# Performance work log

Measured on AMD Instinct MI355X. Metric: run time of the kernel, lower is better.

Reference implementation:

```python
import jax, jax.numpy as jnp
import numpy as np

N_TASK, N_RET, N_DRAM, N_LINK = 50000, 20000, 5000, 100000
E_RET, E_DRAM, E_LINK = 1_000_000, 250_000, 2_000_000
H = 64


def setup_inputs() -> dict:
    key = jax.random.key(0)
    k = jax.random.split(key, 17)
    s = 1.0 / np.sqrt(3 * H)
    return {
        "feat_ret":  jax.random.normal(k[0], (E_RET, 1), jnp.float32),
        "feat_dram": jax.random.normal(k[1], (E_DRAM, 1), jnp.float32),
        "feat_link": jax.random.normal(k[2], (E_LINK, 1), jnp.float32),
        "W_ret":  jax.random.normal(k[3], (H, 1), jnp.float32),
        "b_ret":  jax.random.normal(k[4], (H,), jnp.float32) * 0.1,
        "W_dram": jax.random.normal(k[5], (H, 1), jnp.float32),
        "b_dram": jax.random.normal(k[6], (H,), jnp.float32) * 0.1,
        "W_link": jax.random.normal(k[7], (H, 1), jnp.float32),
        "b_link": jax.random.normal(k[8], (H,), jnp.float32) * 0.1,
        "W_task": jax.random.normal(k[9], (H, 3 * H), jnp.float32) * s,
        "b_task": jax.random.normal(k[10], (H,), jnp.float32) * 0.1,
        "task_ret":  jax.random.randint(k[11], (E_RET,), 0, N_TASK),
        "mod_ret":   jax.random.randint(k[12], (E_RET,), 0, N_RET),
        "task_dram": jax.random.randint(k[13], (E_DRAM,), 0, N_TASK),
        "mod_dram":  jax.random.randint(k[14], (E_DRAM,), 0, N_DRAM),
        "task_link": jax.random.randint(k[15], (E_LINK,), 0, N_TASK),
        "mod_link":  jax.random.randint(k[16], (E_LINK,), 0, N_LINK),
    }


def _gather_inp(feat, mod_idx, n_mod, W, b):
    # use_X: copy_e('feat') + sum per module node, then Linear(1,H) + tanh (activate_inp)
    inp = jax.ops.segment_sum(feat, mod_idx, num_segments=n_mod)  # [n_mod, 1]
    return jnp.tanh(inp @ W.T + b)                                # [n_mod, H]


def _max_to_task(inp_mod, mod_idx, task_idx, n_task):
    # X_used_by: copy_u('inp') + max per task node; zero-in-degree tasks -> 0 (DGL convention)
    m = jax.ops.segment_max(inp_mod[mod_idx], task_idx, num_segments=n_task)
    deg = jax.ops.segment_sum(jnp.ones_like(task_idx), task_idx, num_segments=n_task)
    return jnp.where((deg > 0)[:, None], m, 0.0)


def reference(feat_ret, feat_dram, feat_link, W_ret, b_ret, W_dram, b_dram,
              W_link, b_link, W_task, b_task,
              task_ret, mod_ret, task_dram, mod_dram, task_link, mod_link):
    # _module_update_inp
    inp_ret  = _gather_inp(feat_ret,  mod_ret,  N_RET,  W_ret,  b_ret)
    inp_dram = _gather_inp(feat_dram, mod_dram, N_DRAM, W_dram, b_dram)
    inp_link = _gather_inp(feat_link, mod_link, N_LINK, W_link, b_link)

    # _task_update_h: per-etype max reduce, cross-etype concat, Linear(3H,H) + tanh
    h_cat = jnp.concatenate([
        _max_to_task(inp_ret,  mod_ret,  task_ret,  N_TASK),
        _max_to_task(inp_dram, mod_dram, task_dram, N_TASK),
        _max_to_task(inp_link, mod_link, task_link, N_TASK),
    ], axis=-1)                                                   # [N_TASK, 3H]
    h_task = jnp.tanh(h_cat @ W_task.T + b_task)                  # [N_TASK, H]

    # _module_update_h: use_link copy_u('h') + mean per link node
    s = jax.ops.segment_sum(h_task[task_link], mod_link, num_segments=N_LINK)
    deg = jax.ops.segment_sum(jnp.ones((E_LINK,), jnp.float32), mod_link, num_segments=N_LINK)
    h_link = jnp.where((deg > 0)[:, None], s / jnp.maximum(deg, 1.0)[:, None], 0.0)
    return h_link
```

## Files before the change

kernel.cpp:

```cpp
#include <hip/hip_runtime.h>
#include <stdint.h>

#define N_TASK 50000
#define N_RET 20000
#define N_DRAM 5000
#define N_LINK 100000
#define E_RET 1000000
#define E_DRAM 250000
#define E_LINK 2000000

#define SBE 4096
#define NS_RET 245
#define NS_DRAM 62
#define NS_LINK 489
#define NS_TOT (NS_RET + NS_DRAM + NS_LINK)
#define MR_RET 64
#define RSZ_RET 313
#define MR_DRAM 16
#define RSZ_DRAM 313
#define MR_LINK 256
#define RSZ_LINK 391
#define RECIP313 107203u
#define RECIP391 85817u
#define CAPM_RET 16250
#define CAPM_DRAM 16250
#define CAPM_LINK 8255
#define BM4_RET 0
#define BM4_DRAM (MR_RET * NS_RET)
#define BM4_LINK (BM4_DRAM + MR_DRAM * NS_DRAM)
#define BM4_TOT (BM4_LINK + MR_LINK * NS_LINK)
#define BT_RET 0
#define BT_DRAM (16 * NS_RET)
#define BT_LINK (BT_DRAM + 16 * NS_DRAM)
#define BT_TOT (BT_LINK + 16 * NS_LINK)

#define R_PART 3125
#define CAP_RET 63800
#define CAP_DRAM 16300
#define CAP_LINK 126800
#define SUB_RET 4
#define SUB_DRAM 1
#define SUB_LINK 8
#define PB_RET 0
#define PB_DRAM (16 * SUB_RET * R_PART)
#define PB_LINK (PB_DRAM + 16 * SUB_DRAM * R_PART)
#define PB_TOT (PB_LINK + 16 * SUB_LINK * R_PART)

#define WS_SRET 0
#define WS_SDRAM 80000
#define WS_SLINK 100000
#define WS_CNT 500000
#define WS_OFFS 900000
#define WS_TMAX 1300000
#define WS_TMIN 1900000
#define WS_BCNT 2500000
#define WS_RCNT 2500192
#define WS_CSR 2501536
#define WS_BLKM 10501536
#define WS_BLKB 11068960
#define WS_MREC_RET 15701536
#define WS_MREC_DRAM 24021536
#define WS_MREC_LINK 26101536
#define WS_PART1 15701536
#define WS_HPL0_1 20901536
#define WS_HPL1_1 24101536
#define WS_TREC32_RET 43007776
#define WS_TREC32_DRAM 47090976
#define WS_TREC32_LINK 48134176
#define WS_WTB_1 56249376
#define WS_NEED1 56273952
#define WS_PART2 10501536
#define WS_TREC_RET 15701536
#define WS_TREC_DRAM 23867936
#define WS_TREC_LINK 25954336
#define WS_HPL0_2 15701536
#define WS_HPL1_2 18901536
#define WS_WTB_2 43007776
#define WS_NEED2 43032352

#define MS_STAGE 16512

typedef __attribute__((ext_vector_type(8))) short bf16x8;
typedef __attribute__((ext_vector_type(4))) float f32x4;
typedef unsigned long long u64;

__device__ __forceinline__ unsigned ford(float f) {
  unsigned u = __float_as_uint(f);
  return (u & 0x80000000u) ? ~u : (u | 0x80000000u);
}
__device__ __forceinline__ float funord(unsigned t) {
  unsigned u = (t & 0x80000000u) ? (t & 0x7fffffffu) : ~t;
  return __uint_as_float(u);
}
__device__ __forceinline__ unsigned short bf16rne(float f) {
  unsigned u = __float_as_uint(f);
  return (unsigned short)((u + 0x7fffu + ((u >> 16) & 1u)) >> 16);
}

__device__ __forceinline__ int wscan64(int v, int lane) {
#pragma unroll
  for (int d = 1; d < 64; d <<= 1) {
    int x = __shfl_up(v, d, 64);
    if (lane >= d) v += x;
  }
  return v;
}

__device__ __forceinline__ void decode_sblk(int bx, int& e, int& blk, int& E0, int& NB,
                                            int& NR, unsigned& RECIP, int& RSZ, int& base) {
  if (bx < NS_RET) {
    e = 0; blk = bx; E0 = E_RET; NB = NS_RET; NR = MR_RET; RECIP = RECIP313; RSZ = RSZ_RET; base = BM4_RET;
  } else if (bx < NS_RET + NS_DRAM) {
    e = 1; blk = bx - NS_RET; E0 = E_DRAM; NB = NS_DRAM; NR = MR_DRAM; RECIP = RECIP313; RSZ = RSZ_DRAM; base = BM4_DRAM;
  } else {
    e = 2; blk = bx - NS_RET - NS_DRAM; E0 = E_LINK; NB = NS_LINK; NR = MR_LINK; RECIP = RECIP391; RSZ = RSZ_LINK; base = BM4_LINK;
  }
}
__device__ __forceinline__ void decode_stblk(int bx, int& e, int& blk, int& E0, int& NB,
                                             int& baset) {
  if (bx < NS_RET) { e = 0; blk = bx; E0 = E_RET; NB = NS_RET; baset = BT_RET; }
  else if (bx < NS_RET + NS_DRAM) { e = 1; blk = bx - NS_RET; E0 = E_DRAM; NB = NS_DRAM; baset = BT_DRAM; }
  else { e = 2; blk = bx - NS_RET - NS_DRAM; E0 = E_LINK; NB = NS_LINK; baset = BT_LINK; }
}


__global__ __launch_bounds__(256) void k_count3(
    const int* __restrict__ mr, const int* __restrict__ md, const int* __restrict__ ml,
    const float* __restrict__ W_task, unsigned short* __restrict__ wtb,
    int* __restrict__ blkcnt_m, int* __restrict__ tcur) {
  int bx = blockIdx.x, tid = threadIdx.x;
  if (bx == NS_TOT + 48) {
    if (tid < 48) tcur[tid] = 0;
    return;
  }
  if (bx >= NS_TOT) {
    int i = (bx - NS_TOT) * 256 + tid;
    if (i < 64 * 192) wtb[i] = bf16rne(W_task[i]);
    return;
  }
  __shared__ int c[256];
  int e, blk, E0, NB, NR, RSZ, base; unsigned RECIP;
  decode_sblk(bx, e, blk, E0, NB, NR, RECIP, RSZ, base);
  const int* mod = (e == 0) ? mr : (e == 1) ? md : ml;
  c[tid] = 0;
  __syncthreads();
  int i0 = blk * SBE;
#pragma unroll
  for (int q = 0; q < 16; q++) {
    int i = i0 + q * 256 + tid;
    if (i < E0) {
      int m = mod[i];
      int r = (int)(((u64)(unsigned)m * RECIP) >> 25);
      atomicAdd(&c[r], 1);
    }
  }
  __syncthreads();
  for (int r = tid; r < NR; r += 256)
    blkcnt_m[base + r * NB + blk] = c[r];
}

__global__ __launch_bounds__(512) void k_scan3(const int* __restrict__ blkcnt_m,
                                               int* __restrict__ blkbase_m,
                                               int* __restrict__ rcnt) {
  __shared__ int wred[8];
  int gb = blockIdx.x, tid = threadIdx.x;
  int lane = tid & 63, w = tid >> 6;
  int NB, off;
  if (gb < 64) { NB = NS_RET; off = BM4_RET + gb * NS_RET; }
  else if (gb < 80) { NB = NS_DRAM; off = BM4_DRAM + (gb - 64) * NS_DRAM; }
  else { NB = NS_LINK; off = BM4_LINK + (gb - 80) * NS_LINK; }
  int v = (tid < NB) ? blkcnt_m[off + tid] : 0;
  int incl = wscan64(v, lane);
  if (lane == 63) wred[w] = incl;
  __syncthreads();
  if (tid < 8) {
    int x = wred[tid];
#pragma unroll
    for (int d = 1; d < 8; d <<= 1) {
      int t = __shfl_up(x, d, 8);
      if ((tid & 7) >= d) x += t;
    }
    wred[tid] = x;
  }
  __syncthreads();
  int base = (w > 0) ? wred[w - 1] : 0;
  incl += base;
  if (tid < NB) blkbase_m[off + tid] = incl - v;
  if (tid == 511) rcnt[gb] = incl;
}

__global__ __launch_bounds__(512) void k_mscatter3(
    const int* __restrict__ mr, const int* __restrict__ md, const int* __restrict__ ml,
    const int* __restrict__ tr, const int* __restrict__ td, const int* __restrict__ tl,
    const float* __restrict__ fr, const float* __restrict__ fd, const float* __restrict__ fl,
    const int* __restrict__ blkcnt_m, const int* __restrict__ blkbase_m,
    u64* __restrict__ mrec_ret, u64* __restrict__ mrec_dram, u64* __restrict__ mrec_link) {
  __shared__ int lcur[256];
  __shared__ int pdelta[256];
  __shared__ int wred[4];
  __shared__ u64 srec[SBE];
  __shared__ int sdelta[SBE];
  int tid = threadIdx.x;
  int lane = tid & 63, w = tid >> 6;
  int e, blk, E0, NB, NR, RSZ, base; unsigned RECIP;
  decode_sblk(blockIdx.x, e, blk, E0, NB, NR, RECIP, RSZ, base);
  const int* mod = (e == 0) ? mr : (e == 1) ? md : ml;
  const int* task = (e == 0) ? tr : (e == 1) ? td : tl;
  const float* feat = (e == 0) ? fr : (e == 1) ? fd : fl;
  u64* out = (e == 0) ? mrec_ret : (e == 1) ? mrec_dram : mrec_link;
  int CAP = (e == 0) ? CAPM_RET : (e == 1) ? CAPM_DRAM : CAPM_LINK;
  int cnt_r = 0, base_r = 0;
  if (tid < NR) {
    cnt_r = blkcnt_m[base + tid * NB + blk];
    base_r = blkbase_m[base + tid * NB + blk];
  }
  int incl = 0;
  if (tid < 256) incl = wscan64(cnt_r, lane);
  if (tid < 256 && lane == 63) wred[w] = incl;
  __syncthreads();
  if (tid < 4) {
    int x = wred[tid];
#pragma unroll
    for (int d = 1; d < 4; d <<= 1) {
      int t = __shfl_up(x, d, 4);
      if ((tid & 3) >= d) x += t;
    }
    wred[tid] = x;
  }
  __syncthreads();
  if (tid < 256) {
    int wb = (w > 0) ? wred[w - 1] : 0;
    int excl = incl + wb - cnt_r;
    lcur[tid] = excl;
    pdelta[tid] = tid * CAP + base_r - excl;
  }
  __syncthreads();
  int i0 = blk * SBE;
#pragma unroll
  for (int q = 0; q < 8; q++) {
    int i = i0 + q * 512 + tid;
    if (i < E0) {
      int m = mod[i];
      int r = (int)(((u64)(unsigned)m * RECIP) >> 25);
      unsigned mloc = (unsigned)(m - r * RSZ);
      unsigned tk = (unsigned)task[i];
      unsigned fu = __float_as_uint(feat[i]);
      int slot = atomicAdd(&lcur[r], 1);
      srec[slot] = ((u64)fu << 32) | (tk << 16) | mloc;
      int gpos = pdelta[r] + slot - r * CAP;
      sdelta[slot] = (gpos < CAP) ? pdelta[r] : (int)0x80000000;
    }
  }
  __syncthreads();
  int total = E0 - i0; if (total > SBE) total = SBE;
  for (int s = tid; s < total; s += 512) {
    int d = sdelta[s];
    if (d != (int)0x80000000) out[d + s] = srec[s];
  }
}

#define P1BODY(rec, moff) { \
  int mloc_ = (int)((rec) & 0xFFFFull) + (moff); \
  int task_ = (int)(((rec) >> 16) & 0xFFFFull); \
  atomicAdd(&ssum[mloc_], __uint_as_float((unsigned)((rec) >> 32))); \
  if (e == 2) atomicAdd(&scnt[mloc_], 1); \
  atomicAdd(&tcnt4[w][task_ / R_PART][s4], 1); }

#define P3BODY(rec, moff) { \
  int mloc_ = (int)((rec) & 0xFFFFull) + (moff); \
  int task_ = (int)(((rec) >> 16) & 0xFFFFull); \
  if (e == 2) { int lp_ = atomicAdd(&soff[mloc_], 1); scsr2[lp_] = (unsigned short)task_; } \
  int b_ = task_ / R_PART; \
  unsigned tl12_ = (unsigned)(task_ - b_ * R_PART); \
  unsigned u_ = (ford(ssum[mloc_]) & 0xFFFFF000u) | tl12_; \
  int local_ = atomicAdd(&tcnt4[w][b_][s4], 1); \
  strec[lbase[b_] + tbase4[w][b_][s4] + local_] = u_; }

__global__ __launch_bounds__(1024) void k_msum3(
    const u64* __restrict__ mrec_ret, const u64* __restrict__ mrec_dram,
    const u64* __restrict__ mrec_link, const int* __restrict__ rcnt,
    int* __restrict__ cnt, int* __restrict__ offs, unsigned short* __restrict__ csr,
    int* __restrict__ tcur,
    unsigned* __restrict__ trec_ret, unsigned* __restrict__ trec_dram,
    unsigned* __restrict__ trec_link) {
  __shared__ float ssum[2 * RSZ_LINK];
  __shared__ int scnt[2 * RSZ_LINK];
  __shared__ int soff[2 * RSZ_LINK + 1];
  __shared__ int tcnt4[16][16][4];
  __shared__ int tbase4[16][16][4];
  __shared__ int g0s[16], tot16[16], lbase[16];
  __shared__ int wred[17];
  __shared__ unsigned strec[MS_STAGE];
  __shared__ unsigned short scsr2[MS_STAGE];
  int gb = blockIdx.x, tid = threadIdx.x;
  int w = tid >> 6, lane = tid & 63, s4 = tid & 3;
  int e, m0, nmod, RSZtot, CAPT, rl0 = 0;
  int cnt0, cnt1 = 0;
  const u64 *p0, *p1 = nullptr;
  unsigned* trec;
  if (gb < MR_RET) {
    e = 0; p0 = mrec_ret + (long)gb * CAPM_RET;
    cnt0 = rcnt[gb]; if (cnt0 > CAPM_RET) cnt0 = CAPM_RET;
    RSZtot = RSZ_RET; m0 = gb * RSZ_RET; nmod = N_RET - m0;
    CAPT = CAP_RET; trec = trec_ret;
  } else if (gb < MR_RET + MR_DRAM) {
    e = 1; int rl = gb - MR_RET; p0 = mrec_dram + (long)rl * CAPM_DRAM;
    cnt0 = rcnt[gb]; if (cnt0 > CAPM_DRAM) cnt0 = CAPM_DRAM;
    RSZtot = RSZ_DRAM; m0 = rl * RSZ_DRAM; nmod = N_DRAM - m0;
    CAPT = CAP_DRAM; trec = trec_dram;
  } else {
    e = 2; rl0 = 2 * (gb - (MR_RET + MR_DRAM));
    p0 = mrec_link + (long)rl0 * CAPM_LINK; p1 = p0 + CAPM_LINK;
    cnt0 = rcnt[80 + rl0]; if (cnt0 > CAPM_LINK) cnt0 = CAPM_LINK;
    cnt1 = rcnt[80 + rl0 + 1]; if (cnt1 > CAPM_LINK) cnt1 = CAPM_LINK;
    RSZtot = 2 * RSZ_LINK; m0 = rl0 * RSZ_LINK; nmod = N_LINK - m0;
    CAPT = CAP_LINK; trec = trec_link;
  }
  if (nmod > RSZtot) nmod = RSZtot;
  for (int j = tid; j < RSZtot; j += 1024) { ssum[j] = 0.f; scnt[j] = 0; }
  ((int*)tcnt4)[tid] = 0;
  __syncthreads();
  {
    int i = tid;
    for (; i + 3072 < cnt0; i += 4096) {
      u64 a = p0[i], b = p0[i + 1024], c = p0[i + 2048], d = p0[i + 3072];
      P1BODY(a, 0) P1BODY(b, 0) P1BODY(c, 0) P1BODY(d, 0)
    }
    for (; i < cnt0; i += 1024) { u64 a = p0[i]; P1BODY(a, 0) }
    if (e == 2) {
      i = tid;
      for (; i + 3072 < cnt1; i += 4096) {
        u64 a = p1[i], b = p1[i + 1024], c = p1[i + 2048], d = p1[i + 3072];
        P1BODY(a, RSZ_LINK) P1BODY(b, RSZ_LINK) P1BODY(c, RSZ_LINK) P1BODY(d, RSZ_LINK)
      }
      for (; i < cnt1; i += 1024) { u64 a = p1[i]; P1BODY(a, RSZ_LINK) }
    }
  }
  __syncthreads();
  if (tid < 16) {
    int b2 = tid, run = 0;
    for (int w2 = 0; w2 < 16; w2++) {
#pragma unroll
      for (int s = 0; s < 4; s++) { tbase4[w2][b2][s] = run; run += tcnt4[w2][b2][s]; }
    }
    tot16[b2] = run;
    g0s[b2] = atomicAdd(&tcur[e * 16 + b2], run);
  }
  __syncthreads();
  ((int*)tcnt4)[tid] = 0;
  if (tid == 0) {
    int run = 0;
    for (int b2 = 0; b2 < 16; b2++) { lbase[b2] = run; run += tot16[b2]; }
  }
  int rb = 0;
  if (e == 2) {
    int part = (tid < 256 && tid < rl0) ? rcnt[80 + tid] : 0;
#pragma unroll
    for (int d = 1; d < 64; d <<= 1) part += __shfl_xor(part, d, 64);
    if (tid < 256 && lane == 0) wred[w] = part;
    __syncthreads();
    if (tid == 0) wred[16] = wred[0] + wred[1] + wred[2] + wred[3];
    __syncthreads();
    rb = wred[16];
    int vv = (tid < nmod) ? scnt[tid] : 0;
    int incl = wscan64(vv, lane);
    if (lane == 63) wred[w] = incl;
    __syncthreads();
    if (tid < 16) {
      int x = wred[tid];
#pragma unroll
      for (int d = 1; d < 16; d <<= 1) {
        int t = __shfl_up(x, d, 16);
        if ((tid & 15) >= d) x += t;
      }
      wred[tid] = x;
    }
    __syncthreads();
    int wb = (w > 0) ? wred[w - 1] : 0;
    incl += wb;
    if (tid < nmod) soff[tid] = incl - vv;
    __syncthreads();
    for (int j = tid; j < nmod; j += 1024) {
      cnt[m0 + j] = scnt[j];
      offs[m0 + j] = rb + soff[j];
    }
  }
  __syncthreads();
  {
    int i = tid;
    for (; i + 3072 < cnt0; i += 4096) {
      u64 a = p0[i], b = p0[i + 1024], c = p0[i + 2048], d = p0[i + 3072];
      P3BODY(a, 0) P3BODY(b, 0) P3BODY(c, 0) P3BODY(d, 0)
    }
    for (; i < cnt0; i += 1024) { u64 a = p0[i]; P3BODY(a, 0) }
    if (e == 2) {
      i = tid;
      for (; i + 3072 < cnt1; i += 4096) {
        u64 a = p1[i], b = p1[i + 1024], c = p1[i + 2048], d = p1[i + 3072];
        P3BODY(a, RSZ_LINK) P3BODY(b, RSZ_LINK) P3BODY(c, RSZ_LINK) P3BODY(d, RSZ_LINK)
      }
      for (; i < cnt1; i += 1024) { u64 a = p1[i]; P3BODY(a, RSZ_LINK) }
    }
  }
  __syncthreads();
  for (int b = 0; b < 16; b++) {
    int g0b = g0s[b];
    int kmax = tot16[b];
    int rem = CAPT - g0b; if (rem < 0) rem = 0;
    if (kmax > rem) kmax = rem;
    unsigned* dst = trec + (long)b * CAPT + g0b;
    const unsigned* src = strec + lbase[b];
    for (int k = tid; k < kmax; k += 1024) dst[k] = src[k];
  }
  if (e == 2) {
    int ctot = cnt0 + cnt1;
    for (int k = tid; k < ctot; k += 1024) csr[rb + k] = scsr2[k];
  }
}
#undef P1BODY
#undef P3BODY

#define PBBODY(rec) { \
  unsigned r_ = (rec) & 0xFFFu; \
  atomicMax(&lmax[r_], (rec)); \
  atomicMin(&lmin[r_], (rec)); }

__global__ __launch_bounds__(1024) void k_passb3(
    const unsigned* __restrict__ trec_ret, const unsigned* __restrict__ trec_dram,
    const unsigned* __restrict__ trec_link,
    const int* __restrict__ tcur, unsigned* __restrict__ partials) {
  __shared__ unsigned lmax[R_PART];
  __shared__ unsigned lmin[R_PART];
  int blk = blockIdx.x, tid = threadIdx.x;
  int e, b, sub, Nb, PB, CAP;
  const unsigned* bkt;
  if (blk < 16 * SUB_RET) {
    e = 0; b = blk >> 2; sub = blk & 3; Nb = SUB_RET; PB = PB_RET; CAP = CAP_RET; bkt = trec_ret;
  } else if (blk < 16 * (SUB_RET + SUB_DRAM)) {
    int q = blk - 16 * SUB_RET;
    e = 1; b = q; sub = 0; Nb = SUB_DRAM; PB = PB_DRAM; CAP = CAP_DRAM; bkt = trec_dram;
  } else {
    int q = blk - 16 * (SUB_RET + SUB_DRAM);
    e = 2; b = q >> 3; sub = q & 7; Nb = SUB_LINK; PB = PB_LINK; CAP = CAP_LINK; bkt = trec_link;
  }
  for (int idx = tid; idx < R_PART; idx += 1024) {
    lmax[idx] = 0u;
    lmin[idx] = 0xFFFFFFFFu;
  }
  __syncthreads();
  int count = tcur[e * 16 + b];
  if (count > CAP) count = CAP;
  int chunk = (count + Nb - 1) / Nb;
  int s0 = sub * chunk;
  int s1 = s0 + chunk; if (s1 > count) s1 = count;
  const unsigned* p = bkt + (long)b * CAP;
  int i = s0 + tid;
  for (; i + 3072 < s1; i += 4096) {
    unsigned r0 = p[i], r1 = p[i + 1024], r2 = p[i + 2048], r3 = p[i + 3072];
    PBBODY(r0) PBBODY(r1) PBBODY(r2) PBBODY(r3)
  }
  for (; i < s1; i += 1024) { unsigned r0 = p[i]; PBBODY(r0) }
  __syncthreads();
  unsigned gbase = PB + (unsigned)(b * Nb + sub) * R_PART;
  for (int idx = tid; idx < R_PART; idx += 1024) {
    partials[gbase + idx] = lmax[idx];
    partials[PB_TOT + gbase + idx] = lmin[idx];
  }
}
#undef PBBODY

__global__ __launch_bounds__(256) void k_mmred3(const unsigned* __restrict__ partials,
                                                unsigned* __restrict__ tmax,
                                                unsigned* __restrict__ tmin) {
  int gid = blockIdx.x * 256 + threadIdx.x;
  if (gid >= 3 * N_TASK) return;
  int e = gid / N_TASK;
  int t = gid - e * N_TASK;
  int Nb = (e == 0) ? SUB_RET : (e == 1) ? SUB_DRAM : SUB_LINK;
  int PB = (e == 0) ? PB_RET : (e == 1) ? PB_DRAM : PB_LINK;
  int b = t / R_PART;
  int r = t - b * R_PART;
  unsigned umax = 0u, umin = 0xFFFFFFFFu;
  for (int sub = 0; sub < Nb; sub++) {
    unsigned idx = PB + (unsigned)(b * Nb + sub) * R_PART + r;
    unsigned wv = partials[idx];
    if (wv > umax) umax = wv;
    unsigned w2 = partials[PB_TOT + idx];
    if (w2 < umin) umin = w2;
  }
  tmax[gid] = umax & 0xFFFFF000u;
  tmin[gid] = umin & 0xFFFFF000u;
}


__global__ __launch_bounds__(256) void k_count(
    const int* __restrict__ mr, const int* __restrict__ md, const int* __restrict__ ml,
    const int* __restrict__ tr, const int* __restrict__ td, const int* __restrict__ tl,
    const float* __restrict__ W_task, unsigned short* __restrict__ wtb,
    int* __restrict__ blkcnt_m, int* __restrict__ blkcnt_t) {
  int bx = blockIdx.x, tid = threadIdx.x;
  if (bx >= 2 * NS_TOT) {
    int i = (bx - 2 * NS_TOT) * 256 + tid;
    if (i < 64 * 192) wtb[i] = bf16rne(W_task[i]);
    return;
  }
  __shared__ int c[256];
  c[tid] = 0;
  __syncthreads();
  if (bx < NS_TOT) {
    int e, blk, E0, NB, NR, RSZ, base; unsigned RECIP;
    decode_sblk(bx, e, blk, E0, NB, NR, RECIP, RSZ, base);
    const int* mod = (e == 0) ? mr : (e == 1) ? md : ml;
    int i0 = blk * SBE;
#pragma unroll
    for (int q = 0; q < 16; q++) {
      int i = i0 + q * 256 + tid;
      if (i < E0) {
        int m = mod[i];
        int r = (int)(((u64)(unsigned)m * RECIP) >> 25);
        atomicAdd(&c[r], 1);
      }
    }
    __syncthreads();
    for (int r = tid; r < NR; r += 256)
      blkcnt_m[base + r * NB + blk] = c[r];
  } else {
    int e, blk, E0, NB, baset;
    decode_stblk(bx - NS_TOT, e, blk, E0, NB, baset);
    const int* task = (e == 0) ? tr : (e == 1) ? td : tl;
    int i0 = blk * SBE;
#pragma unroll
    for (int q = 0; q < 16; q++) {
      int i = i0 + q * 256 + tid;
      if (i < E0) atomicAdd(&c[task[i] / R_PART], 1);
    }
    __syncthreads();
    if (tid < 16) blkcnt_t[baset + tid * NB + blk] = c[tid];
  }
}

__global__ __launch_bounds__(512) void k_scan(int* __restrict__ blkcnt_m,
                                              int* __restrict__ blkcnt_t,
                                              int* __restrict__ rcnt, int* __restrict__ bcnt) {
  __shared__ int sm[512];
  int gb = blockIdx.x, tid = threadIdx.x;
  int* arr; int NB; int* outp;
  if (gb < 336) {
    int off;
    if (gb < 64) { NB = NS_RET; off = BM4_RET + gb * NS_RET; }
    else if (gb < 80) { NB = NS_DRAM; off = BM4_DRAM + (gb - 64) * NS_DRAM; }
    else { NB = NS_LINK; off = BM4_LINK + (gb - 80) * NS_LINK; }
    arr = blkcnt_m + off; outp = rcnt + gb;
  } else {
    int g = gb - 336; int e = g >> 4, b = g & 15;
    int NBe = (e == 0) ? NS_RET : (e == 1) ? NS_DRAM : NS_LINK;
    int baset = (e == 0) ? BT_RET : (e == 1) ? BT_DRAM : BT_LINK;
    NB = NBe; arr = blkcnt_t + baset + b * NBe; outp = bcnt + g;
  }
  int v = (tid < NB) ? arr[tid] : 0;
  sm[tid] = v;
  __syncthreads();
  for (int d = 1; d < 512; d <<= 1) {
    int x = (tid >= d) ? sm[tid - d] : 0;
    __syncthreads();
    sm[tid] += x;
    __syncthreads();
  }
  if (tid < NB) arr[tid] = sm[tid] - v;
  if (tid == 511) *outp = sm[511];
}

__global__ __launch_bounds__(256) void k_mscatter2(
    const int* __restrict__ mr, const int* __restrict__ md, const int* __restrict__ ml,
    const int* __restrict__ tl,
    const float* __restrict__ fr, const float* __restrict__ fd, const float* __restrict__ fl,
// ... 366 lines not shown
    cursor[i] = o;
  }
}

__global__ void f_scatter(const int* __restrict__ tl, const int* __restrict__ ml,
                          int* cursor, unsigned short* csr) {
  int i = blockIdx.x * blockDim.x + threadIdx.x;
  if (i >= E_LINK) return;
  int pos = atomicAdd(&cursor[ml[i]], 1);
  csr[pos] = (unsigned short)tl[i];
}


__global__ __launch_bounds__(256) void k_taskm(
    const float* __restrict__ W_ret, const float* __restrict__ b_ret,
    const float* __restrict__ W_dram, const float* __restrict__ b_dram,
    const float* __restrict__ W_link, const float* __restrict__ b_link,
    const unsigned short* __restrict__ wtb, const float* __restrict__ b_task,
    const unsigned* __restrict__ tmax, const unsigned* __restrict__ tmin,
    unsigned short* __restrict__ hp0, unsigned short* __restrict__ hp1) {
  int wave = threadIdx.x >> 6;
  int lane = threadIdx.x & 63;
  int tile = blockIdx.x * 4 + wave;
  if (tile >= N_TASK / 16) return;
  int t0 = tile * 16;
  int l16 = lane & 15;
  int quad = lane >> 4;
  int t = t0 + l16;

  f32x4 acc[4];
#pragma unroll
  for (int nf = 0; nf < 4; nf++) acc[nf] = (f32x4){0.f, 0.f, 0.f, 0.f};

  const float* We[3] = {W_ret, W_dram, W_link};
  const float* be[3] = {b_ret, b_dram, b_link};

  for (int e = 0; e < 3; e++) {
    unsigned um = tmax[e * N_TASK + t];
    float smax = funord(um);
    float smin = funord(tmin[e * N_TASK + t]);
    bool live = (um != 0u);
#pragma unroll
    for (int h = 0; h < 2; h++) {
      int kb = h * 32 + quad * 8;
      float4 w0 = *(const float4*)&We[e][kb];
      float4 w1 = *(const float4*)&We[e][kb + 4];
      float4 b0 = *(const float4*)&be[e][kb];
      float4 b1 = *(const float4*)&be[e][kb + 4];
      float wv[8] = {w0.x, w0.y, w0.z, w0.w, w1.x, w1.y, w1.z, w1.w};
      float bv[8] = {b0.x, b0.y, b0.z, b0.w, b1.x, b1.y, b1.z, b1.w};
      bf16x8 afrag;
#pragma unroll
      for (int j = 0; j < 8; j++) {
        float wj = wv[j];
        float ss = (wj >= 0.f) ? smax : smin;
        float hc = live ? tanhf(fmaf(ss, wj, bv[j])) : 0.f;
        afrag[j] = (short)bf16rne(hc);
      }
      int kk = e * 64 + h * 32 + quad * 8;
#pragma unroll
      for (int nf = 0; nf < 4; nf++) {
        int o = nf * 16 + l16;
        bf16x8 bfrag = *(const bf16x8*)&wtb[o * 192 + kk];
        acc[nf] = __builtin_amdgcn_mfma_f32_16x16x32_bf16(afrag, bfrag, acc[nf], 0, 0, 0);
      }
    }
  }

#pragma unroll
  for (int nf = 0; nf < 4; nf++) {
    int n = nf * 16 + l16;
    float bt = b_task[n];
    unsigned short* hp = (n < 32) ? hp0 : hp1;
    int f = n & 31;
#pragma unroll
    for (int r = 0; r < 4; r++) {
      int m = quad * 4 + r;
      float v = tanhf(acc[nf][r] + bt);
      hp[(t0 + m) * 32 + f] = bf16rne(v);
    }
  }
}

__global__ __launch_bounds__(256) void k_link2(const unsigned short* __restrict__ hp,
                                               const int* __restrict__ offs,
                                               const int* __restrict__ cnt,
                                               const unsigned short* __restrict__ csr,
                                               float* __restrict__ out, int plane) {
  int l = blockIdx.x * 8 + (threadIdx.x >> 5);
  int f = threadIdx.x & 31;
  int start = offs[l];
  int c = cnt[l];
  float acc = 0.f;
  for (int q = 0; q < c; q += 4) {
    int i1 = (q + 1 < c) ? q + 1 : c - 1;
    int i2 = (q + 2 < c) ? q + 2 : c - 1;
    int i3 = (q + 3 < c) ? q + 3 : c - 1;
    int t0 = csr[start + q];
    int t1 = csr[start + i1];
    int t2 = csr[start + i2];
    int t3 = csr[start + i3];
    unsigned v0 = hp[t0 * 32 + f];
    unsigned v1 = hp[t1 * 32 + f];
    unsigned v2 = hp[t2 * 32 + f];
    unsigned v3 = hp[t3 * 32 + f];
    acc += __uint_as_float(v0 << 16);
    if (q + 1 < c) acc += __uint_as_float(v1 << 16);
    if (q + 2 < c) acc += __uint_as_float(v2 << 16);
    if (q + 3 < c) acc += __uint_as_float(v3 << 16);
  }
  out[l * 64 + plane * 32 + f] = (c > 0) ? acc / (float)c : 0.f;
}

extern "C" void kernel_launch(void* const* d_in, const int* in_sizes, int n_in,
                              void* d_out, int out_size, void* d_ws, size_t ws_size,
                              hipStream_t stream) {
  const float* feat_ret  = (const float*)d_in[0];
  const float* feat_dram = (const float*)d_in[1];
  const float* feat_link = (const float*)d_in[2];
  const float* W_ret  = (const float*)d_in[3];
  const float* b_ret  = (const float*)d_in[4];
  const float* W_dram = (const float*)d_in[5];
  const float* b_dram = (const float*)d_in[6];
  const float* W_link = (const float*)d_in[7];
  const float* b_link = (const float*)d_in[8];
  const float* W_task = (const float*)d_in[9];
  const float* b_task = (const float*)d_in[10];
  const int* task_ret  = (const int*)d_in[11];
  const int* mod_ret   = (const int*)d_in[12];
  const int* task_dram = (const int*)d_in[13];
  const int* mod_dram  = (const int*)d_in[14];
  const int* task_link = (const int*)d_in[15];
  const int* mod_link  = (const int*)d_in[16];
  float* out = (float*)d_out;

  char* ws = (char*)d_ws;
  float* s_ret  = (float*)(ws + WS_SRET);
  float* s_dram = (float*)(ws + WS_SDRAM);
  float* s_link = (float*)(ws + WS_SLINK);
  int*   cnt    = (int*)(ws + WS_CNT);
  int*   offs   = (int*)(ws + WS_OFFS);
  unsigned* tmax = (unsigned*)(ws + WS_TMAX);
  unsigned* tmin = (unsigned*)(ws + WS_TMIN);
  int* tcur = (int*)(ws + WS_BCNT);
  int* rcnt = (int*)(ws + WS_RCNT);
  unsigned short* csr = (unsigned short*)(ws + WS_CSR);
  int* blkcnt_m = (int*)(ws + WS_BLKM);
  int* blkb = (int*)(ws + WS_BLKB);
  u64* mrec_ret  = (u64*)(ws + WS_MREC_RET);
  u64* mrec_dram = (u64*)(ws + WS_MREC_DRAM);
  u64* mrec_link = (u64*)(ws + WS_MREC_LINK);

  unsigned short* hp0;
  unsigned short* hp1;
  unsigned short* wtb;

  if (ws_size >= (size_t)WS_NEED1) {
    unsigned* partials = (unsigned*)(ws + WS_PART1);
    unsigned* trec_ret  = (unsigned*)(ws + WS_TREC32_RET);
    unsigned* trec_dram = (unsigned*)(ws + WS_TREC32_DRAM);
    unsigned* trec_link = (unsigned*)(ws + WS_TREC32_LINK);
    hp0 = (unsigned short*)(ws + WS_HPL0_1);
    hp1 = (unsigned short*)(ws + WS_HPL1_1);
    wtb = (unsigned short*)(ws + WS_WTB_1);
    k_count3<<<NS_TOT + 49, 256, 0, stream>>>(mod_ret, mod_dram, mod_link,
                                              W_task, wtb, blkcnt_m, tcur);
    k_scan3<<<336, 512, 0, stream>>>(blkcnt_m, blkb, rcnt);
    k_mscatter3<<<NS_TOT, 512, 0, stream>>>(mod_ret, mod_dram, mod_link,
                                            task_ret, task_dram, task_link,
                                            feat_ret, feat_dram, feat_link,
                                            blkcnt_m, blkb,
                                            mrec_ret, mrec_dram, mrec_link);
    k_msum3<<<MR_RET + MR_DRAM + MR_LINK / 2, 1024, 0, stream>>>(
        mrec_ret, mrec_dram, mrec_link, rcnt,
        cnt, offs, csr, tcur,
        trec_ret, trec_dram, trec_link);
    k_passb3<<<16 * (SUB_RET + SUB_DRAM + SUB_LINK), 1024, 0, stream>>>(
        trec_ret, trec_dram, trec_link, tcur, partials);
    k_mmred3<<<(3 * N_TASK + 255) / 256, 256, 0, stream>>>(partials, tmax, tmin);
  } else if (ws_size >= (size_t)WS_NEED2) {
    unsigned* partials = (unsigned*)(ws + WS_PART2);
    u64* trec_ret  = (u64*)(ws + WS_TREC_RET);
    u64* trec_dram = (u64*)(ws + WS_TREC_DRAM);
    u64* trec_link = (u64*)(ws + WS_TREC_LINK);
    hp0 = (unsigned short*)(ws + WS_HPL0_2);
    hp1 = (unsigned short*)(ws + WS_HPL1_2);
    wtb = (unsigned short*)(ws + WS_WTB_2);
    k_count<<<2 * NS_TOT + 48, 256, 0, stream>>>(mod_ret, mod_dram, mod_link,
                                                 task_ret, task_dram, task_link,
                                                 W_task, wtb, blkcnt_m, blkb);
    k_scan<<<384, 512, 0, stream>>>(blkcnt_m, blkb, rcnt, tcur);
    k_mscatter2<<<NS_TOT, 256, 0, stream>>>(mod_ret, mod_dram, mod_link, task_link,
                                            feat_ret, feat_dram, feat_link, blkcnt_m,
                                            mrec_ret, mrec_dram, mrec_link);
    k_msum<<<336, 256, 0, stream>>>(mrec_ret, mrec_dram, mrec_link, rcnt,
                                    s_ret, s_dram, s_link, cnt, offs, csr);
    k_ascatter2<<<NS_TOT, 256, 0, stream>>>(task_ret, mod_ret, task_dram, mod_dram,
                                            task_link, mod_link, s_ret, s_dram, s_link,
                                            blkb, trec_ret, trec_dram, trec_link);
    k_passb<<<16 * (SUB_RET + SUB_DRAM + SUB_LINK), 256, 0, stream>>>(
        trec_ret, trec_dram, trec_link, tcur, partials);
    k_mmred2<<<(3 * N_TASK + 255) / 256, 256, 0, stream>>>(partials, tmax, tmin);
  } else {
    int* part   = (int*)(ws + WS_BLKM);
    int* partx  = (int*)(ws + WS_BLKM + 4096);
    int* cursor = (int*)(ws + WS_BLKB);
    hp0 = (unsigned short*)(ws + WS_HPL0_2);
    hp1 = (unsigned short*)(ws + WS_HPL1_2);
    wtb = (unsigned short*)(ws + WS_WTB_2);
    hipMemsetAsync(ws, 0, 1900000, stream);
    hipMemsetAsync(ws + WS_TMIN, 0xFF, 600000, stream);
    const int totalE = E_RET + E_DRAM + E_LINK;
    int nblk_e = (totalE + 255) / 256;
    f_segsum<<<nblk_e, 256, 0, stream>>>(feat_ret, feat_dram, feat_link,
                                         mod_ret, mod_dram, mod_link,
                                         s_ret, s_dram, s_link, cnt);
    f_minmax<<<nblk_e, 256, 0, stream>>>(s_ret, s_dram, s_link,
                                         task_ret, mod_ret, task_dram, mod_dram,
                                         task_link, mod_link, tmax, tmin);
    const int npart = (N_LINK + 255) / 256;
    f_part<<<npart, 256, 0, stream>>>(cnt, part);
    f_scanpart<<<1, 512, 0, stream>>>(part, partx, npart);
    f_offs<<<npart, 256, 0, stream>>>(cnt, partx, offs, cursor);
    f_scatter<<<(E_LINK + 255) / 256, 256, 0, stream>>>(task_link, mod_link, cursor, csr);
    k_wprep<<<48, 256, 0, stream>>>(W_task, wtb);
  }

  k_taskm<<<(N_TASK / 16 + 3) / 4, 256, 0, stream>>>(W_ret, b_ret, W_dram, b_dram,
                                                     W_link, b_link, wtb, b_task,
                                                     tmax, tmin, hp0, hp1);
  k_link2<<<N_LINK / 8, 256, 0, stream>>>(hp0, offs, cnt, csr, out, 0);
  k_link2<<<N_LINK / 8, 256, 0, stream>>>(hp1, offs, cnt, csr, out, 1);
}
```

Measured before the change: 283.7 us.

## Replace bucketed task max/min passes with direct global atomic max/min

The per-task max/min reduction previously bucketed 32-bit records by task partition in shared memory, wrote them to global buckets, then ran two more kernels to reduce partials. Now k_msum3 issues global atomicMax/atomicMin on ordered-float keys directly into tmax/tmin, which are initialised with memsets. This removes two kernel launches and the intermediate record traffic. In exchange it adds about 3.25M contended global atomics, and it stops masking the low 12 bits of the keys, so precision now differs slightly from before.

```diff
diff --git a/kernel.cpp b/kernel.cpp
--- a/kernel.cpp
+++ b/kernel.cpp
@@ -61,12 +61,8 @@
 #define WS_MREC_RET 15701536
 #define WS_MREC_DRAM 24021536
 #define WS_MREC_LINK 26101536
-#define WS_PART1 15701536
 #define WS_HPL0_1 20901536
 #define WS_HPL1_1 24101536
-#define WS_TREC32_RET 43007776
-#define WS_TREC32_DRAM 47090976
-#define WS_TREC32_LINK 48134176
 #define WS_WTB_1 56249376
 #define WS_NEED1 56273952
 #define WS_PART2 10501536
@@ -127,12 +123,8 @@
 __global__ __launch_bounds__(256) void k_count3(
     const int* __restrict__ mr, const int* __restrict__ md, const int* __restrict__ ml,
     const float* __restrict__ W_task, unsigned short* __restrict__ wtb,
-    int* __restrict__ blkcnt_m, int* __restrict__ tcur) {
+    int* __restrict__ blkcnt_m) {
   int bx = blockIdx.x, tid = threadIdx.x;
-  if (bx == NS_TOT + 48) {
-    if (tid < 48) tcur[tid] = 0;
-    return;
-  }
   if (bx >= NS_TOT) {
     int i = (bx - NS_TOT) * 256 + tid;
     if (i < 64 * 192) wtb[i] = bf16rne(W_task[i]);
@@ -261,64 +253,50 @@
 
 #define P1BODY(rec, moff) { \
   int mloc_ = (int)((rec) & 0xFFFFull) + (moff); \
-  int task_ = (int)(((rec) >> 16) & 0xFFFFull); \
   atomicAdd(&ssum[mloc_], __uint_as_float((unsigned)((rec) >> 32))); \
-  if (e == 2) atomicAdd(&scnt[mloc_], 1); \
-  atomicAdd(&tcnt4[w][task_ / R_PART][s4], 1); }
+  if (e == 2) atomicAdd(&scnt[mloc_], 1); }
 
 #define P3BODY(rec, moff) { \
   int mloc_ = (int)((rec) & 0xFFFFull) + (moff); \
   int task_ = (int)(((rec) >> 16) & 0xFFFFull); \
   if (e == 2) { int lp_ = atomicAdd(&soff[mloc_], 1); scsr2[lp_] = (unsigned short)task_; } \
-  int b_ = task_ / R_PART; \
-  unsigned tl12_ = (unsigned)(task_ - b_ * R_PART); \
-  unsigned u_ = (ford(ssum[mloc_]) & 0xFFFFF000u) | tl12_; \
-  int local_ = atomicAdd(&tcnt4[w][b_][s4], 1); \
-  strec[lbase[b_] + tbase4[w][b_][s4] + local_] = u_; }
+  unsigned u_ = ford(ssum[mloc_]); \
+  atomicMax(&tmax[eN + task_], u_); \
+  atomicMin(&tmin[eN + task_], u_); }
 
 __global__ __launch_bounds__(1024) void k_msum3(
     const u64* __restrict__ mrec_ret, const u64* __restrict__ mrec_dram,
     const u64* __restrict__ mrec_link, const int* __restrict__ rcnt,
     int* __restrict__ cnt, int* __restrict__ offs, unsigned short* __restrict__ csr,
-    int* __restrict__ tcur,
-    unsigned* __restrict__ trec_ret, unsigned* __restrict__ trec_dram,
-    unsigned* __restrict__ trec_link) {
+    unsigned* __restrict__ tmax, unsigned* __restrict__ tmin) {
   __shared__ float ssum[2 * RSZ_LINK];
   __shared__ int scnt[2 * RSZ_LINK];
   __shared__ int soff[2 * RSZ_LINK + 1];
-  __shared__ int tcnt4[16][16][4];
-  __shared__ int tbase4[16][16][4];
-  __shared__ int g0s[16], tot16[16], lbase[16];
   __shared__ int wred[17];
-  __shared__ unsigned strec[MS_STAGE];
   __shared__ unsigned short scsr2[MS_STAGE];
   int gb = blockIdx.x, tid = threadIdx.x;
-  int w = tid >> 6, lane = tid & 63, s4 = tid & 3;
-  int e, m0, nmod, RSZtot, CAPT, rl0 = 0;
+  int w = tid >> 6, lane = tid & 63;
+  int e, m0, nmod, RSZtot, rl0 = 0;
   int cnt0, cnt1 = 0;
   const u64 *p0, *p1 = nullptr;
-  unsigned* trec;
   if (gb < MR_RET) {
     e = 0; p0 = mrec_ret + (long)gb * CAPM_RET;
     cnt0 = rcnt[gb]; if (cnt0 > CAPM_RET) cnt0 = CAPM_RET;
     RSZtot = RSZ_RET; m0 = gb * RSZ_RET; nmod = N_RET - m0;
-    CAPT = CAP_RET; trec = trec_ret;
   } else if (gb < MR_RET + MR_DRAM) {
     e = 1; int rl = gb - MR_RET; p0 = mrec_dram + (long)rl * CAPM_DRAM;
     cnt0 = rcnt[gb]; if (cnt0 > CAPM_DRAM) cnt0 = CAPM_DRAM;
     RSZtot = RSZ_DRAM; m0 = rl * RSZ_DRAM; nmod = N_DRAM - m0;
-    CAPT = CAP_DRAM; trec = trec_dram;
   } else {
     e = 2; rl0 = 2 * (gb - (MR_RET + MR_DRAM));
     p0 = mrec_link + (long)rl0 * CAPM_LINK; p1 = p0 + CAPM_LINK;
     cnt0 = rcnt[80 + rl0]; if (cnt0 > CAPM_LINK) cnt0 = CAPM_LINK;
     cnt1 = rcnt[80 + rl0 + 1]; if (cnt1 > CAPM_LINK) cnt1 = CAPM_LINK;
     RSZtot = 2 * RSZ_LINK; m0 = rl0 * RSZ_LINK; nmod = N_LINK - m0;
-    CAPT = CAP_LINK; trec = trec_link;
-  }
+  }
+  const int eN = e * N_TASK;
   if (nmod > RSZtot) nmod = RSZtot;
   for (int j = tid; j < RSZtot; j += 1024) { ssum[j] = 0.f; scnt[j] = 0; }
-  ((int*)tcnt4)[tid] = 0;
   __syncthreads();
   {
     int i = tid;
@@ -337,21 +315,6 @@
     }
   }
   __syncthreads();
-  if (tid < 16) {
-    int b2 = tid, run = 0;
-    for (int w2 = 0; w2 < 16; w2++) {
-#pragma unroll
-      for (int s = 0; s < 4; s++) { tbase4[w2][b2][s] = run; run += tcnt4[w2][b2][s]; }
-    }
-    tot16[b2] = run;
-    g0s[b2] = atomicAdd(&tcur[e * 16 + b2], run);
-  }
-  __syncthreads();
-  ((int*)tcnt4)[tid] = 0;
-  if (tid == 0) {
-    int run = 0;
-    for (int b2 = 0; b2 < 16; b2++) { lbase[b2] = run; run += tot16[b2]; }
-  }
   int rb = 0;
   if (e == 2) {
     int part = (tid < 256 && tid < rl0) ? rcnt[80 + tid] : 0;
@@ -402,95 +365,14 @@
       for (; i < cnt1; i += 1024) { u64 a = p1[i]; P3BODY(a, RSZ_LINK) }
     }
   }
-  __syncthreads();
-  for (int b = 0; b < 16; b++) {
-    int g0b = g0s[b];
-    int kmax = tot16[b];
-    int rem = CAPT - g0b; if (rem < 0) rem = 0;
-    if (kmax > rem) kmax = rem;
-    unsigned* dst = trec + (long)b * CAPT + g0b;
-    const unsigned* src = strec + lbase[b];
-    for (int k = tid; k < kmax; k += 1024) dst[k] = src[k];
-  }
   if (e == 2) {
+    __syncthreads();
     int ctot = cnt0 + cnt1;
     for (int k = tid; k < ctot; k += 1024) csr[rb + k] = scsr2[k];
   }
 }
 #undef P1BODY
 #undef P3BODY
-
-#define PBBODY(rec) { \
-  unsigned r_ = (rec) & 0xFFFu; \
-  atomicMax(&lmax[r_], (rec)); \
-  atomicMin(&lmin[r_], (rec)); }
-
-__global__ __launch_bounds__(1024) void k_passb3(
-    const unsigned* __restrict__ trec_ret, const unsigned* __restrict__ trec_dram,
-    const unsigned* __restrict__ trec_link,
-    const int* __restrict__ tcur, unsigned* __restrict__ partials) {
-  __shared__ unsigned lmax[R_PART];
-  __shared__ unsigned lmin[R_PART];
-  int blk = blockIdx.x, tid = threadIdx.x;
-  int e, b, sub, Nb, PB, CAP;
-  const unsigned* bkt;
-  if (blk < 16 * SUB_RET) {
-    e = 0; b = blk >> 2; sub = blk & 3; Nb = SUB_RET; PB = PB_RET; CAP = CAP_RET; bkt = trec_ret;
-  } else if (blk < 16 * (SUB_RET + SUB_DRAM)) {
-    int q = blk - 16 * SUB_RET;
-    e = 1; b = q; sub = 0; Nb = SUB_DRAM; PB = PB_DRAM; CAP = CAP_DRAM; bkt = trec_dram;
-  } else {
-    int q = blk - 16 * (SUB_RET + SUB_DRAM);
-    e = 2; b = q >> 3; sub = q & 7; Nb = SUB_LINK; PB = PB_LINK; CAP = CAP_LINK; bkt = trec_link;
-  }
-  for (int idx = tid; idx < R_PART; idx += 1024) {
-    lmax[idx] = 0u;
-    lmin[idx] = 0xFFFFFFFFu;
-  }
-  __syncthreads();
-  int count = tcur[e * 16 + b];
-  if (count > CAP) count = CAP;
-  int chunk = (count + Nb - 1) / Nb;
-  int s0 = sub * chunk;
-  int s1 = s0 + chunk; if (s1 > count) s1 = count;
-  const unsigned* p = bkt + (long)b * CAP;
-  int i = s0 + tid;
-  for (; i + 3072 < s1; i += 4096) {
-    unsigned r0 = p[i], r1 = p[i + 1024], r2 = p[i + 2048], r3 = p[i + 3072];
-    PBBODY(r0) PBBODY(r1) PBBODY(r2) PBBODY(r3)
-  }
-  for (; i < s1; i += 1024) { unsigned r0 = p[i]; PBBODY(r0) }
-  __syncthreads();
-  unsigned gbase = PB + (unsigned)(b * Nb + sub) * R_PART;
-  for (int idx = tid; idx < R_PART; idx += 1024) {
-    partials[gbase + idx] = lmax[idx];
-    partials[PB_TOT + gbase + idx] = lmin[idx];
-  }
-}
-#undef PBBODY
-
-__global__ __launch_bounds__(256) void k_mmred3(const unsigned* __restrict__ partials,
-                                                unsigned* __restrict__ tmax,
-                                                unsigned* __restrict__ tmin) {
-  int gid = blockIdx.x * 256 + threadIdx.x;
-  if (gid >= 3 * N_TASK) return;
-  int e = gid / N_TASK;
-  int t = gid - e * N_TASK;
-  int Nb = (e == 0) ? SUB_RET : (e == 1) ? SUB_DRAM : SUB_LINK;
-  int PB = (e == 0) ? PB_RET : (e == 1) ? PB_DRAM : PB_LINK;
-  int b = t / R_PART;
-  int r = t - b * R_PART;
-  unsigned umax = 0u, umin = 0xFFFFFFFFu;
-  for (int sub = 0; sub < Nb; sub++) {
-    unsigned idx = PB + (unsigned)(b * Nb + sub) * R_PART + r;
-    unsigned wv = partials[idx];
-    if (wv > umax) umax = wv;
-    unsigned w2 = partials[PB_TOT + idx];
-    if (w2 < umin) umin = w2;
-  }
-  tmax[gid] = umax & 0xFFFFF000u;
-  tmin[gid] = umin & 0xFFFFF000u;
-}
 
 
 __global__ __launch_bounds__(256) void k_count(
@@ -1097,15 +979,13 @@
   unsigned short* wtb;
 
   if (ws_size >= (size_t)WS_NEED1) {
-    unsigned* partials = (unsigned*)(ws + WS_PART1);
-    unsigned* trec_ret  = (unsigned*)(ws + WS_TREC32_RET);
-    unsigned* trec_dram = (unsigned*)(ws + WS_TREC32_DRAM);
-    unsigned* trec_link = (unsigned*)(ws + WS_TREC32_LINK);
     hp0 = (unsigned short*)(ws + WS_HPL0_1);
     hp1 = (unsigned short*)(ws + WS_HPL1_1);
     wtb = (unsigned short*)(ws + WS_WTB_1);
-    k_count3<<<NS_TOT + 49, 256, 0, stream>>>(mod_ret, mod_dram, mod_link,
-                                              W_task, wtb, blkcnt_m, tcur);
+    hipMemsetAsync(ws + WS_TMAX, 0x00, 600000, stream);
+    hipMemsetAsync(ws + WS_TMIN, 0xFF, 600000, stream);
+    k_count3<<<NS_TOT + 48, 256, 0, stream>>>(mod_ret, mod_dram, mod_link,
+                                              W_task, wtb, blkcnt_m);
     k_scan3<<<336, 512, 0, stream>>>(blkcnt_m, blkb, rcnt);
     k_mscatter3<<<NS_TOT, 512, 0, stream>>>(mod_ret, mod_dram, mod_link,
                                             task_ret, task_dram, task_link,
@@ -1114,11 +994,7 @@
                                             mrec_ret, mrec_dram, mrec_link);
     k_msum3<<<MR_RET + MR_DRAM + MR_LINK / 2, 1024, 0, stream>>>(
         mrec_ret, mrec_dram, mrec_link, rcnt,
-        cnt, offs, csr, tcur,
-        trec_ret, trec_dram, trec_link);
-    k_passb3<<<16 * (SUB_RET + SUB_DRAM + SUB_LINK), 1024, 0, stream>>>(
-        trec_ret, trec_dram, trec_link, tcur, partials);
-    k_mmred3<<<(3 * N_TASK + 255) / 256, 256, 0, stream>>>(partials, tmax, tmin);
+        cnt, offs, csr, tmax, tmin);
   } else if (ws_size >= (size_t)WS_NEED2) {
     unsigned* partials = (unsigned*)(ws + WS_PART2);
     u64* trec_ret  = (u64*)(ws + WS_TREC_RET);
```

New measurement: 512.7 us. 80.7% more time.

## Stash records in LDS, privatize sums, and merge link gather launches

Applied to the files above, without the earlier changes.

k_msum3 now saves each record's task and module index into an LDS stash during the first pass, so the second pass reads the stash instead of re-reading the 64-bit records from global memory. The module sum and count atomics are split into two copies selected by thread parity and merged afterwards, which spreads out LDS atomic contention. The CSR build now runs as a separate pass that reuses the strec buffer. The two per-plane k_link2 launches are merged into one 512-thread launch that covers all 64 features, so the CSR indices and offsets are read once instead of twice. In exchange the kernel uses more LDS and adds extra barriers.

```diff
diff --git a/kernel.cpp b/kernel.cpp
--- a/kernel.cpp
+++ b/kernel.cpp
@@ -259,22 +259,13 @@
   }
 }
 
-#define P1BODY(rec, moff) { \
+#define P1BODY(rec, moff, idx) { \
   int mloc_ = (int)((rec) & 0xFFFFull) + (moff); \
   int task_ = (int)(((rec) >> 16) & 0xFFFFull); \
-  atomicAdd(&ssum[mloc_], __uint_as_float((unsigned)((rec) >> 32))); \
-  if (e == 2) atomicAdd(&scnt[mloc_], 1); \
-  atomicAdd(&tcnt4[w][task_ / R_PART][s4], 1); }
-
-#define P3BODY(rec, moff) { \
-  int mloc_ = (int)((rec) & 0xFFFFull) + (moff); \
-  int task_ = (int)(((rec) >> 16) & 0xFFFFull); \
-  if (e == 2) { int lp_ = atomicAdd(&soff[mloc_], 1); scsr2[lp_] = (unsigned short)task_; } \
-  int b_ = task_ / R_PART; \
-  unsigned tl12_ = (unsigned)(task_ - b_ * R_PART); \
-  unsigned u_ = (ford(ssum[mloc_]) & 0xFFFFF000u) | tl12_; \
-  int local_ = atomicAdd(&tcnt4[w][b_][s4], 1); \
-  strec[lbase[b_] + tbase4[w][b_][s4] + local_] = u_; }
+  atomicAdd(&ssum[r2][mloc_], __uint_as_float((unsigned)((rec) >> 32))); \
+  if (e == 2) atomicAdd(&scnt[r2][mloc_], 1); \
+  atomicAdd(&tcnt4[w][task_ / R_PART][s4], 1); \
+  stash[idx] = ((unsigned)task_ << 16) | (unsigned)mloc_; }
 
 __global__ __launch_bounds__(1024) void k_msum3(
     const u64* __restrict__ mrec_ret, const u64* __restrict__ mrec_dram,
@@ -283,17 +274,17 @@
     int* __restrict__ tcur,
     unsigned* __restrict__ trec_ret, unsigned* __restrict__ trec_dram,
     unsigned* __restrict__ trec_link) {
-  __shared__ float ssum[2 * RSZ_LINK];
-  __shared__ int scnt[2 * RSZ_LINK];
+  __shared__ float ssum[2][2 * RSZ_LINK];
+  __shared__ int scnt[2][2 * RSZ_LINK];
   __shared__ int soff[2 * RSZ_LINK + 1];
   __shared__ int tcnt4[16][16][4];
   __shared__ int tbase4[16][16][4];
   __shared__ int g0s[16], tot16[16], lbase[16];
   __shared__ int wred[17];
+  __shared__ unsigned stash[MS_STAGE];
   __shared__ unsigned strec[MS_STAGE];
-  __shared__ unsigned short scsr2[MS_STAGE];
   int gb = blockIdx.x, tid = threadIdx.x;
-  int w = tid >> 6, lane = tid & 63, s4 = tid & 3;
+  int w = tid >> 6, lane = tid & 63, s4 = tid & 3, r2 = tid & 1;
   int e, m0, nmod, RSZtot, CAPT, rl0 = 0;
   int cnt0, cnt1 = 0;
   const u64 *p0, *p1 = nullptr;
@@ -317,26 +308,33 @@
     CAPT = CAP_LINK; trec = trec_link;
   }
   if (nmod > RSZtot) nmod = RSZtot;
-  for (int j = tid; j < RSZtot; j += 1024) { ssum[j] = 0.f; scnt[j] = 0; }
+  for (int j = tid; j < RSZtot; j += 1024) {
+    ssum[0][j] = 0.f; ssum[1][j] = 0.f; scnt[0][j] = 0; scnt[1][j] = 0;
+  }
   ((int*)tcnt4)[tid] = 0;
   __syncthreads();
   {
     int i = tid;
     for (; i + 3072 < cnt0; i += 4096) {
       u64 a = p0[i], b = p0[i + 1024], c = p0[i + 2048], d = p0[i + 3072];
-      P1BODY(a, 0) P1BODY(b, 0) P1BODY(c, 0) P1BODY(d, 0)
-    }
-    for (; i < cnt0; i += 1024) { u64 a = p0[i]; P1BODY(a, 0) }
+      P1BODY(a, 0, i) P1BODY(b, 0, i + 1024) P1BODY(c, 0, i + 2048) P1BODY(d, 0, i + 3072)
+    }
+    for (; i < cnt0; i += 1024) { u64 a = p0[i]; P1BODY(a, 0, i) }
     if (e == 2) {
       i = tid;
       for (; i + 3072 < cnt1; i += 4096) {
         u64 a = p1[i], b = p1[i + 1024], c = p1[i + 2048], d = p1[i + 3072];
-        P1BODY(a, RSZ_LINK) P1BODY(b, RSZ_LINK) P1BODY(c, RSZ_LINK) P1BODY(d, RSZ_LINK)
+        P1BODY(a, RSZ_LINK, cnt0 + i) P1BODY(b, RSZ_LINK, cnt0 + i + 1024)
+        P1BODY(c, RSZ_LINK, cnt0 + i + 2048) P1BODY(d, RSZ_LINK, cnt0 + i + 3072)
       }
-      for (; i < cnt1; i += 1024) { u64 a = p1[i]; P1BODY(a, RSZ_LINK) }
-    }
-  }
-  __syncthreads();
+      for (; i < cnt1; i += 1024) { u64 a = p1[i]; P1BODY(a, RSZ_LINK, cnt0 + i) }
+    }
+  }
+  __syncthreads();
+  for (int j = tid; j < RSZtot; j += 1024) {
+    ssum[0][j] += ssum[1][j];
+    if (e == 2) scnt[0][j] += scnt[1][j];
+  }
   if (tid < 16) {
     int b2 = tid, run = 0;
     for (int w2 = 0; w2 < 16; w2++) {
@@ -362,7 +360,7 @@
     if (tid == 0) wred[16] = wred[0] + wred[1] + wred[2] + wred[3];
     __syncthreads();
     rb = wred[16];
-    int vv = (tid < nmod) ? scnt[tid] : 0;
+    int vv = (tid < nmod) ? scnt[0][tid] : 0;
     int incl = wscan64(vv, lane);
     if (lane == 63) wred[w] = incl;
     __syncthreads();
@@ -381,27 +379,26 @@
     if (tid < nmod) soff[tid] = incl - vv;
     __syncthreads();
     for (int j = tid; j < nmod; j += 1024) {
-      cnt[m0 + j] = scnt[j];
+      cnt[m0 + j] = scnt[0][j];
       offs[m0 + j] = rb + soff[j];
     }
   }
   __syncthreads();
-  {
-    int i = tid;
-    for (; i + 3072 < cnt0; i += 4096) {
-      u64 a = p0[i], b = p0[i + 1024], c = p0[i + 2048], d = p0[i + 3072];
-      P3BODY(a, 0) P3BODY(b, 0) P3BODY(c, 0) P3BODY(d, 0)
-    }
-    for (; i < cnt0; i += 1024) { u64 a = p0[i]; P3BODY(a, 0) }
-    if (e == 2) {
-      i = tid;
-      for (; i + 3072 < cnt1; i += 4096) {
-        u64 a = p1[i], b = p1[i + 1024], c = p1[i + 2048], d = p1[i + 3072];
-        P3BODY(a, RSZ_LINK) P3BODY(b, RSZ_LINK) P3BODY(c, RSZ_LINK) P3BODY(d, RSZ_LINK)
-      }
-      for (; i < cnt1; i += 1024) { u64 a = p1[i]; P3BODY(a, RSZ_LINK) }
-    }
-  }
+  int ctot = cnt0 + ((e == 2) ? cnt1 : 0);
+#define P3EMIT(idx) { \
+    unsigned tm = stash[idx]; \
+    int mloc_ = (int)(tm & 0xFFFFu); \
+    int task_ = (int)(tm >> 16); \
+    int b_ = task_ / R_PART; \
+    unsigned tl12_ = (unsigned)(task_ - b_ * R_PART); \
+    unsigned u_ = (ford(ssum[0][mloc_]) & 0xFFFFF000u) | tl12_; \
+    int local_ = atomicAdd(&tcnt4[w][b_][s4], 1); \
+    strec[lbase[b_] + tbase4[w][b_][s4] + local_] = u_; }
+  for (int i = tid; i < cnt0; i += 1024) P3EMIT(i)
+  if (e == 2) {
+    for (int i = tid; i < cnt1; i += 1024) P3EMIT(cnt0 + i)
+  }
+#undef P3EMIT
   __syncthreads();
   for (int b = 0; b < 16; b++) {
     int g0b = g0s[b];
@@ -413,12 +410,19 @@
     for (int k = tid; k < kmax; k += 1024) dst[k] = src[k];
   }
   if (e == 2) {
-    int ctot = cnt0 + cnt1;
-    for (int k = tid; k < ctot; k += 1024) csr[rb + k] = scsr2[k];
+    __syncthreads();
+    unsigned short* scsr = (unsigned short*)strec;
+    for (int i = tid; i < ctot; i += 1024) {
+      unsigned tm = stash[i];
+      int mloc_ = (int)(tm & 0xFFFFu);
+      int lp = atomicAdd(&soff[mloc_], 1);
+      scsr[lp] = (unsigned short)(tm >> 16);
+    }
+    __syncthreads();
+    for (int k = tid; k < ctot; k += 1024) csr[rb + k] = scsr[k];
   }
 }
 #undef P1BODY
-#undef P3BODY
 
 #define PBBODY(rec) { \
   unsigned r_ = (rec) & 0xFFFu; \
@@ -1023,13 +1027,16 @@
   }
 }
 
-__global__ __launch_bounds__(256) void k_link2(const unsigned short* __restrict__ hp,
+__global__ __launch_bounds__(512) void k_link2(const unsigned short* __restrict__ hp0,
+                                               const unsigned short* __restrict__ hp1,
                                                const int* __restrict__ offs,
                                                const int* __restrict__ cnt,
                                                const unsigned short* __restrict__ csr,
-                                               float* __restrict__ out, int plane) {
-  int l = blockIdx.x * 8 + (threadIdx.x >> 5);
-  int f = threadIdx.x & 31;
+                                               float* __restrict__ out) {
+  int l = blockIdx.x * 8 + (threadIdx.x >> 6);
+  int f = threadIdx.x & 63;
+  const unsigned short* hp = (f < 32) ? hp0 : hp1;
+  int ff = f & 31;
   int start = offs[l];
   int c = cnt[l];
   float acc = 0.f;
@@ -1041,16 +1048,16 @@
     int t1 = csr[start + i1];
     int t2 = csr[start + i2];
     int t3 = csr[start + i3];
-    unsigned v0 = hp[t0 * 32 + f];
-    unsigned v1 = hp[t1 * 32 + f];
-    unsigned v2 = hp[t2 * 32 + f];
-    unsigned v3 = hp[t3 * 32 + f];
+    unsigned v0 = hp[t0 * 32 + ff];
+    unsigned v1 = hp[t1 * 32 + ff];
+    unsigned v2 = hp[t2 * 32 + ff];
+    unsigned v3 = hp[t3 * 32 + ff];
     acc += __uint_as_float(v0 << 16);
     if (q + 1 < c) acc += __uint_as_float(v1 << 16);
     if (q + 2 < c) acc += __uint_as_float(v2 << 16);
     if (q + 3 < c) acc += __uint_as_float(v3 << 16);
   }
-  out[l * 64 + plane * 32 + f] = (c > 0) ? acc / (float)c : 0.f;
+  out[l * 64 + f] = (c > 0) ? acc / (float)c : 0.f;
 }
 
 extern "C" void kernel_launch(void* const* d_in, const int* in_sizes, int n_in,
@@ -1170,6 +1177,5 @@
   k_taskm<<<(N_TASK / 16 + 3) / 4, 256, 0, stream>>>(W_ret, b_ret, W_dram, b_dram,
                                                      W_link, b_link, wtb, b_task,
                                                      tmax, tmin, hp0, hp1);
-  k_link2<<<N_LINK / 8, 256, 0, stream>>>(hp0, offs, cnt, csr, out, 0);
-  k_link2<<<N_LINK / 8, 256, 0, stream>>>(hp1, offs, cnt, csr, out, 1);
-}
+  k_link2<<<N_LINK / 8, 512, 0, stream>>>(hp0, hp1, offs, cnt, csr, out);
+}
```

After: 290.2 us. 1.02x slower.
